# Kernel tuning notes

Measured on AMD Instinct MI355X. Metric: run time of the kernel, lower is better.

## Reference

```python
import jax, jax.numpy as jnp
import numpy as np

B, NT, NP = 4096, 2048, 1024
DT = 1e-3


def _cum_trap(y, dx):
    # cumulative trapezoid along last dim, zero-prepended (preserve_dims=True)
    c = jnp.cumsum((y[..., 1:] + y[..., :-1]) * (0.5 * dx), axis=-1)
    return jnp.concatenate([jnp.zeros_like(y[..., :1]), c], axis=-1)


def _trapz(y, dx):
    return jnp.sum(y[..., :-1] + y[..., 1:], axis=-1) * (0.5 * dx)


def _renorm(f, dx):
    # square-normalize so each trace integrates to 1 (valid pdf)
    sq = f * f
    return sq / _trapz(sq, dx)[..., None]


def _natural_cubic_coeffs(p, q):
    # p: [NP] uniform knots, q: [B, NP] values -> per-interval coeffs a,b,c,d [B, NP-1]
    h = p[1] - p[0]
    n = p.shape[0]
    rhs = 6.0 * (q[..., :-2] - 2.0 * q[..., 1:-1] + q[..., 2:]) / (h * h)  # [B, n-2]
    m = n - 2
    A = 4.0 * jnp.eye(m, dtype=q.dtype) + jnp.eye(m, k=1, dtype=q.dtype) + jnp.eye(m, k=-1, dtype=q.dtype)
    M_int = jnp.linalg.solve(A, rhs.T).T                      # [B, n-2]
    zero = jnp.zeros_like(q[..., :1])
    M = jnp.concatenate([zero, M_int, zero], axis=-1)          # natural BC: M0 = Mn = 0
    a = q[..., :-1]
    b = (q[..., 1:] - q[..., :-1]) / h - h * (2.0 * M[..., :-1] + M[..., 1:]) / 6.0
    c = M[..., :-1] / 2.0
    d = (M[..., 1:] - M[..., :-1]) / (6.0 * h)
    return a, b, c, d


def _spline_eval(p, coeffs, x):
    # evaluate batched natural cubic splines at x: [B, NT]
    a, b, c, d = coeffs
    idx = jnp.clip(jnp.searchsorted(p, x, side='right') - 1, 0, p.shape[0] - 2)  # [B, NT]
    s = x - p[idx]
    ag = jnp.take_along_axis(a, idx, axis=-1)
    bg = jnp.take_along_axis(b, idx, axis=-1)
    cg = jnp.take_along_axis(c, idx, axis=-1)
    dg = jnp.take_along_axis(d, idx, axis=-1)
    return ag + s * (bg + s * (cg + s * dg))


def setup_inputs() -> dict:
    key = jax.random.key(0)
    k1, k2 = jax.random.split(key)
    f = jax.random.normal(k1, (B, NT), dtype=jnp.float32)
    obs_data = jax.random.normal(k2, (B, NT), dtype=jnp.float32)
    t = jnp.arange(NT, dtype=jnp.float32) * DT
    p = jnp.linspace(0.0, 1.0, NP, dtype=jnp.float32)
    return {"f": f, "obs_data": obs_data, "t": t, "p": p}


def reference(f, obs_data, t, p):
    dt = t[1] - t[0]
    # ---- __init__: build per-trace quantile splines from obs_data ----
    obs_tilde = _renorm(obs_data, dt)                 # [B, NT] pdf
    cdf_obs = _cum_trap(obs_tilde, dt)                # [B, NT] cdf
    # true_quantile: step lookup q(p) = t[searchsorted(cdf, p)]
    idx = jax.vmap(lambda c: jnp.searchsorted(c, p))(cdf_obs)
    idx = jnp.clip(idx, 0, t.shape[0] - 1)
    q = t[idx]                                        # [B, NP]
    coeffs = _natural_cubic_coeffs(p, q)
    # ---- forward: W2 distance ----
    f_tilde = _renorm(f, dt)                          # [B, NT]
    F = _cum_trap(f_tilde, dt)                        # [B, NT] cdf of f
    off_diag = _spline_eval(p, coeffs, F)             # Q_obs(F(t)) [B, NT]
    diff = (t[None, :] - off_diag) ** 2
    integrated = _trapz(diff * f_tilde, dt)           # [B]
    return integrated.sum()
```

## Files before the change

kernel.cpp:

```cpp
#include <hip/hip_runtime.h>

#define NBATCH 4096
#define NT 2048
#define NP 1024
#define NTH 256
#define EPT 8
#define PPT 4
#define MSZ 1022
#define KT 4
#define IMGW 14

__global__ __launch_bounds__(NTH, 4) void w2loss_kernel(
    const float* __restrict__ f,
    const float* __restrict__ obs,
    float* __restrict__ partial)
{
    __shared__ float sQ[NP];
    __shared__ float sM[NP];
    __shared__ __align__(16) float sU[4096];
    __shared__ float sH[NTH];
    __shared__ float sPow[IMGW];
    __shared__ float sWSA[4], sWSB[4];
    __shared__ float sSqA[2], sSqB[2];
    __shared__ float sRed[4];

    float* sRp = sU;
    float4* sCF = reinterpret_cast<float4*>(sU);

    const int tid  = threadIdx.x;
    const int lane = tid & 63;
    const int wid  = tid >> 6;
    const int b    = blockIdx.x;
    const int base = tid * EPT;

    const float dt      = 0.001f;
    const float half_dt = 0.0005f;
    const float h       = 0.00097751710654936461f;
    const float inv_h   = 1023.0f;
    const float inv_h2  = 1046529.0f;
    const float h6      = h * (1.0f / 6.0f);
    const float ih6     = inv_h * (1.0f / 6.0f);

    const float* orow = obs + (size_t)b * NT;
    const float* frow = f   + (size_t)b * NT;
    float4 o0 = *reinterpret_cast<const float4*>(orow + base);
    float4 o1 = *reinterpret_cast<const float4*>(orow + base + 4);
    float4 g0 = *reinterpret_cast<const float4*>(frow + base);
    float4 g1 = *reinterpret_cast<const float4*>(frow + base + 4);

    if (tid < IMGW) {
        const float rho = -0.26794919243112270f;
        float v = 1.0f;
        for (int i = 0; i < tid; ++i) v *= rho;
        sPow[tid] = v;
    }
    if (tid < KT) { sRp[tid] = 0.0f; sRp[KT + MSZ + tid] = 0.0f; }

    float prefA[EPT], prefB[EPT];
    {
        float s0;
        s0 = o0.x*o0.x; prefA[0] = s0;
        s0 = o0.y*o0.y; prefA[1] = prefA[0] + s0;
        s0 = o0.z*o0.z; prefA[2] = prefA[1] + s0;
        s0 = o0.w*o0.w; prefA[3] = prefA[2] + s0;
        s0 = o1.x*o1.x; prefA[4] = prefA[3] + s0;
        s0 = o1.y*o1.y; prefA[5] = prefA[4] + s0;
        s0 = o1.z*o1.z; prefA[6] = prefA[5] + s0;
        s0 = o1.w*o1.w; prefA[7] = prefA[6] + s0;
        s0 = g0.x*g0.x; prefB[0] = s0;
        s0 = g0.y*g0.y; prefB[1] = prefB[0] + s0;
        s0 = g0.z*g0.z; prefB[2] = prefB[1] + s0;
        s0 = g0.w*g0.w; prefB[3] = prefB[2] + s0;
        s0 = g1.x*g1.x; prefB[4] = prefB[3] + s0;
        s0 = g1.y*g1.y; prefB[5] = prefB[4] + s0;
        s0 = g1.z*g1.z; prefB[6] = prefB[5] + s0;
        s0 = g1.w*g1.w; prefB[7] = prefB[6] + s0;
    }
    float sqA7 = o1.w * o1.w;
    float sqB7 = g1.w * g1.w;
    sH[tid] = sqA7;

    float tsA = prefA[EPT - 1], tsB = prefB[EPT - 1];
    float wsA = tsA, wsB = tsB;
#pragma unroll
    for (int off = 1; off < 64; off <<= 1) {
        float uA = __shfl_up(wsA, off);
        float uB = __shfl_up(wsB, off);
        if (lane >= off) { wsA += uA; wsB += uB; }
    }
    if (lane == 63) { sWSA[wid] = wsA; sWSB[wid] = wsB; }
    if (tid == 0)       { sSqA[0] = prefA[0]; sSqB[0] = prefB[0]; }
    if (tid == NTH - 1) { sSqA[1] = sqA7;     sSqB[1] = sqB7; }
    __syncthreads();

    float exclA = wsA - tsA, exclB = wsB - tsB;
    if (wid > 0) { exclA += sWSA[0]; exclB += sWSB[0]; }
    if (wid > 1) { exclA += sWSA[1]; exclB += sWSB[1]; }
    if (wid > 2) { exclA += sWSA[2]; exclB += sWSB[2]; }
    float totA = sWSA[0] + sWSA[1] + sWSA[2] + sWSA[3];
    float totB = sWSB[0] + sWSB[1] + sWSB[2] + sWSB[3];
    float sq0A = sSqA[0], sq0B = sSqB[0];
    float invSA = 1.0f / (half_dt * (2.0f * totA - sSqA[1] - sq0A));
    float invSB = 1.0f / (half_dt * (2.0f * totB - sSqB[1] - sq0B));

    {
        float cm;
        if (tid == 0) cm = -1.0f;
        else {
            float sqprev = sH[tid - 1];
            cm = half_dt * (((exclA - sqprev) + exclA) - sq0A) * invSA;
        }
        float Pm = exclA;
#pragma unroll
        for (int e = 0; e < EPT; ++e) {
            int j = base + e;
            float Pj = exclA + prefA[e];
            float cc = (j == 0) ? 0.0f : half_dt * (Pm + Pj - sq0A) * invSA;
            int kLo = (int)floorf(cm * inv_h) + 1;
            int kHi = (int)floorf(cc * inv_h);
            if (kLo < 0) kLo = 0;
            if (j == NT - 1) kHi = NP - 1;
            else {
                if (e == EPT - 1) kHi += 1;
                if (kHi > NP - 1) kHi = NP - 1;
            }
            float qv = (float)j * dt;
            for (int k = kLo; k <= kHi; ++k) sQ[k] = qv;
            cm = cc;
            Pm = Pj;
        }
    }
    __syncthreads();

#pragma unroll
    for (int kk = 0; kk < PPT; ++kk) {
        int i = tid + kk * NTH;
        if (i < MSZ)
            sRp[KT + i] = 6.0f * (sQ[i] - 2.0f * sQ[i + 1] + sQ[i + 2]) * inv_h2;
    }
    __syncthreads();

    {
        const float Cg = 0.28867513459481288f;
        const float CP[KT + 1] = {
            1.0f, -0.26794919243112270f, 0.071796769724490830f,
            -0.019237886466840586f, 0.0051547761428899979f };
#pragma unroll
        for (int kk = 0; kk < PPT; ++kk) {
            int i = tid + kk * NTH;
            if (i < MSZ) {
                float acc = 0.0f;
#pragma unroll
                for (int d = -KT; d <= KT; ++d) {
                    int ad = d < 0 ? -d : d;
                    acc += CP[ad] * sRp[KT + i + d];
                }
                if (i + 1 < IMGW) {
                    float t1 = 0.0f;
#pragma unroll
                    for (int k2 = 0; k2 < IMGW - 1; ++k2) t1 += sPow[k2 + 1] * sRp[KT + k2];
                    acc -= sPow[i + 1] * t1;
                }
                if (MSZ - i < IMGW) {
                    float t2 = 0.0f;
#pragma unroll
                    for (int k2 = MSZ - IMGW + 1; k2 < MSZ; ++k2) t2 += sPow[MSZ - k2] * sRp[KT + k2];
                    acc -= sPow[MSZ - i] * t2;
                }
                sM[i + 1] = Cg * acc;
            }
        }
    }
    if (tid == 0) { sM[0] = 0.0f; sM[NP - 1] = 0.0f; }
    __syncthreads();

#pragma unroll
    for (int kk = 0; kk < PPT; ++kk) {
        int k = tid + kk * NTH;
        if (k < NP - 1) {
            float a  = sQ[k];
            float qn = sQ[k + 1];
            float Mk = sM[k];
            float Mn = sM[k + 1];
            float4 cf;
            cf.x = a;
            cf.y = (qn - a) * inv_h - (2.0f * Mk + Mn) * h6;
            cf.z = 0.5f * Mk;
            cf.w = (Mn - Mk) * ih6;
            sCF[k] = cf;
        }
    }
    __syncthreads();

    float local = 0.0f;
    float term0 = 0.0f, term7 = 0.0f;
    {
        const float c1B = half_dt * invSB;
        const float K0  = (2.0f * exclB - sq0B) * c1B;
        float tj = (float)base * dt;
#pragma unroll
        for (int e = 0; e < EPT; ++e) {
            float Gj = (e ? prefB[e - 1] : 0.0f) + prefB[e];
            float Fj = __builtin_fmaf(Gj, c1B, K0);
            float sqe = e ? (prefB[e] - prefB[e - 1]) : prefB[0];
            float kf = Fj * inv_h;
            kf = fminf(fmaxf(kf, 0.0f), 1022.0f);
            int k = (int)kf;
            float s = __builtin_fmaf(-h, (float)k, Fj);
            float4 cf = sCF[k];
            float od = cf.x + s * (cf.y + s * (cf.z + s * cf.w));
            float dd = tj - od;
            float term = dd * dd * sqe;
            local += term;
            if (e == 0) term0 = term;
            if (e == EPT - 1) term7 = term;
            tj += dt;
        }
    }
    if (tid == 0)       local -= 0.5f * term0;
    if (tid == NTH - 1) local -= 0.5f * term7;

#pragma unroll
    for (int off = 32; off > 0; off >>= 1) local += __shfl_down(local, off);
    if (lane == 0) sRed[wid] = local;
    __syncthreads();
    if (tid == 0) partial[b] = (sRed[0] + sRed[1] + sRed[2] + sRed[3]) * (dt * invSB);
}

__global__ __launch_bounds__(NTH) void w2loss_reduce(
    const float* __restrict__ partial, float* __restrict__ out)
{
    __shared__ float sRed[4];
    const int tid  = threadIdx.x;
    const int lane = tid & 63;
    const int wid  = tid >> 6;
    float s = 0.0f;
#pragma unroll
    for (int i = 0; i < 16; i += 4) {
        float4 v = *reinterpret_cast<const float4*>(partial + tid * 16 + i);
        s += v.x + v.y + v.z + v.w;
    }
#pragma unroll
    for (int off = 32; off > 0; off >>= 1) s += __shfl_down(s, off);
    if (lane == 0) sRed[wid] = s;
    __syncthreads();
    if (tid == 0) out[0] = sRed[0] + sRed[1] + sRed[2] + sRed[3];
}

extern "C" void kernel_launch(void* const* d_in, const int* in_sizes, int n_in,
                              void* d_out, int out_size, void* d_ws, size_t ws_size,
                              hipStream_t stream) {
    const float* f   = (const float*)d_in[0];
    const float* obs = (const float*)d_in[1];
    float* out     = (float*)d_out;
    float* partial = (float*)d_ws;

    w2loss_kernel<<<NBATCH, NTH, 0, stream>>>(f, obs, partial);
    w2loss_reduce<<<1, NTH, 0, stream>>>(partial, out);
}
```

Baseline: 29.01 us.

## Fuse spline RHS, solve, and coefficient stages into register-tiled pass

```diff
diff --git a/kernel.cpp b/kernel.cpp
--- a/kernel.cpp
+++ b/kernel.cpp
@@ -5,27 +5,25 @@
 #define NP 1024
 #define NTH 256
 #define EPT 8
-#define PPT 4
 #define MSZ 1022
 #define KT 4
 #define IMGW 14
 
-__global__ __launch_bounds__(NTH, 4) void w2loss_kernel(
+__device__ __forceinline__ int pQ(int x) { return x + (x >> 3) + 9; }
+__device__ __forceinline__ int pM(int x) { return x + (x >> 3); }
+
+__global__ __launch_bounds__(NTH, 2) void w2loss_kernel(
     const float* __restrict__ f,
     const float* __restrict__ obs,
     float* __restrict__ partial)
 {
-    __shared__ float sQ[NP];
-    __shared__ float sM[NP];
-    __shared__ __align__(16) float sU[4096];
+    __shared__ float sQp[1168];
+    __shared__ float sMp[1152];
     __shared__ float sH[NTH];
     __shared__ float sPow[IMGW];
     __shared__ float sWSA[4], sWSB[4];
     __shared__ float sSqA[2], sSqB[2];
     __shared__ float sRed[4];
-
-    float* sRp = sU;
-    float4* sCF = reinterpret_cast<float4*>(sU);
 
     const int tid  = threadIdx.x;
     const int lane = tid & 63;
@@ -54,7 +52,6 @@
         for (int i = 0; i < tid; ++i) v *= rho;
         sPow[tid] = v;
     }
-    if (tid < KT) { sRp[tid] = 0.0f; sRp[KT + MSZ + tid] = 0.0f; }
 
     float prefA[EPT], prefB[EPT];
     {
@@ -125,18 +122,10 @@
                 if (kHi > NP - 1) kHi = NP - 1;
             }
             float qv = (float)j * dt;
-            for (int k = kLo; k <= kHi; ++k) sQ[k] = qv;
+            for (int k = kLo; k <= kHi; ++k) sQp[pQ(k)] = qv;
             cm = cc;
             Pm = Pj;
         }
-    }
-    __syncthreads();
-
-#pragma unroll
-    for (int kk = 0; kk < PPT; ++kk) {
-        int i = tid + kk * NTH;
-        if (i < MSZ)
-            sRp[KT + i] = 6.0f * (sQ[i] - 2.0f * sQ[i + 1] + sQ[i + 2]) * inv_h2;
     }
     __syncthreads();
 
@@ -145,49 +134,56 @@
         const float CP[KT + 1] = {
             1.0f, -0.26794919243112270f, 0.071796769724490830f,
             -0.019237886466840586f, 0.0051547761428899979f };
-#pragma unroll
-        for (int kk = 0; kk < PPT; ++kk) {
-            int i = tid + kk * NTH;
-            if (i < MSZ) {
-                float acc = 0.0f;
-#pragma unroll
-                for (int d = -KT; d <= KT; ++d) {
-                    int ad = d < 0 ? -d : d;
-                    acc += CP[ad] * sRp[KT + i + d];
-                }
-                if (i + 1 < IMGW) {
-                    float t1 = 0.0f;
-#pragma unroll
-                    for (int k2 = 0; k2 < IMGW - 1; ++k2) t1 += sPow[k2 + 1] * sRp[KT + k2];
-                    acc -= sPow[i + 1] * t1;
-                }
-                if (MSZ - i < IMGW) {
-                    float t2 = 0.0f;
-#pragma unroll
-                    for (int k2 = MSZ - IMGW + 1; k2 < MSZ; ++k2) t2 += sPow[MSZ - k2] * sRp[KT + k2];
-                    acc -= sPow[MSZ - i] * t2;
-                }
-                sM[i + 1] = Cg * acc;
-            }
-        }
-    }
-    if (tid == 0) { sM[0] = 0.0f; sM[NP - 1] = 0.0f; }
-    __syncthreads();
-
-#pragma unroll
-    for (int kk = 0; kk < PPT; ++kk) {
-        int k = tid + kk * NTH;
-        if (k < NP - 1) {
-            float a  = sQ[k];
-            float qn = sQ[k + 1];
-            float Mk = sM[k];
-            float Mn = sM[k + 1];
-            float4 cf;
-            cf.x = a;
-            cf.y = (qn - a) * inv_h - (2.0f * Mk + Mn) * h6;
-            cf.z = 0.5f * Mk;
-            cf.w = (Mn - Mk) * ih6;
-            sCF[k] = cf;
+        const int k0 = tid * 4;
+
+        float qw[14];
+#pragma unroll
+        for (int x = 0; x < 14; ++x) qw[x] = sQp[pQ(k0 - 5 + x)];
+
+        float r[12];
+#pragma unroll
+        for (int x = 0; x < 12; ++x) {
+            int gi = k0 - 5 + x;
+            float v = 6.0f * (qw[x] - 2.0f * qw[x + 1] + qw[x + 2]) * inv_h2;
+            r[x] = (gi >= 0 && gi < MSZ) ? v : 0.0f;
+        }
+
+        float T1 = 0.0f, T2 = 0.0f;
+        if (tid < 4) {
+            float qe[15];
+#pragma unroll
+            for (int x = 0; x < 15; ++x) qe[x] = sQp[pQ(x)];
+#pragma unroll
+            for (int x = 0; x < IMGW - 1; ++x) {
+                float rr = 6.0f * (qe[x] - 2.0f * qe[x + 1] + qe[x + 2]) * inv_h2;
+                T1 += sPow[x + 1] * rr;
+            }
+        }
+        if (tid >= NTH - 4) {
+            float qe[15];
+#pragma unroll
+            for (int x = 0; x < 15; ++x) qe[x] = sQp[pQ(1009 + x)];
+#pragma unroll
+            for (int x = 0; x < IMGW - 1; ++x) {
+                float rr = 6.0f * (qe[x] - 2.0f * qe[x + 1] + qe[x + 2]) * inv_h2;
+                T2 += sPow[13 - x] * rr;
+            }
+        }
+
+#pragma unroll
+        for (int e = 0; e < 4; ++e) {
+            int k = k0 + e;
+            float acc = 0.0f;
+#pragma unroll
+            for (int d = -KT; d <= KT; ++d) {
+                int ad = d < 0 ? -d : d;
+                acc += CP[ad] * r[e + 4 + d];
+            }
+            if (k < IMGW)        acc -= sPow[k] * T1;
+            if (1023 - k < IMGW) acc -= sPow[1023 - k] * T2;
+            float mv = Cg * acc;
+            if (k == 0 || k == NP - 1) mv = 0.0f;
+            sMp[pM(k)] = mv;
         }
     }
     __syncthreads();
@@ -207,9 +203,13 @@
             kf = fminf(fmaxf(kf, 0.0f), 1022.0f);
             int k = (int)kf;
             float s = __builtin_fmaf(-h, (float)k, Fj);
-            float4 cf = sCF[k];
-            float od = cf.x + s * (cf.y + s * (cf.z + s * cf.w));
-            float dd = tj - od;
+            float q0 = sQp[pQ(k)];
+            float q1 = sQp[pQ(k + 1)];
+            float M0 = sMp[pM(k)];
+            float M1 = sMp[pM(k + 1)];
+            float bco = (q1 - q0) * inv_h - (2.0f * M0 + M1) * h6;
+            float od  = q0 + s * (bco + s * (0.5f * M0 + s * (M1 - M0) * ih6));
+            float dd  = tj - od;
             float term = dd * dd * sqe;
             local += term;
             if (e == 0) term0 = term;
```

Measured after the change: 32.25 us. 1.11x slower.

## Fuse spline coefficient build into evaluation and pad shared arrays

Applied to the files above, without the earlier changes.

```diff
diff --git a/kernel.cpp b/kernel.cpp
--- a/kernel.cpp
+++ b/kernel.cpp
@@ -10,22 +10,21 @@
 #define KT 4
 #define IMGW 14
 
-__global__ __launch_bounds__(NTH, 4) void w2loss_kernel(
+__device__ __forceinline__ int pI(int x) { return x + (x >> 3); }
+
+__global__ __launch_bounds__(NTH, 8) void w2loss_kernel(
     const float* __restrict__ f,
     const float* __restrict__ obs,
     float* __restrict__ partial)
 {
-    __shared__ float sQ[NP];
-    __shared__ float sM[NP];
-    __shared__ __align__(16) float sU[4096];
+    __shared__ float sQp[1156];
+    __shared__ float sMp[1156];
+    __shared__ float sRp[MSZ + 2 * KT];
     __shared__ float sH[NTH];
     __shared__ float sPow[IMGW];
     __shared__ float sWSA[4], sWSB[4];
     __shared__ float sSqA[2], sSqB[2];
     __shared__ float sRed[4];
-
-    float* sRp = sU;
-    float4* sCF = reinterpret_cast<float4*>(sU);
 
     const int tid  = threadIdx.x;
     const int lane = tid & 63;
@@ -125,7 +124,7 @@
                 if (kHi > NP - 1) kHi = NP - 1;
             }
             float qv = (float)j * dt;
-            for (int k = kLo; k <= kHi; ++k) sQ[k] = qv;
+            for (int k = kLo; k <= kHi; ++k) sQp[pI(k)] = qv;
             cm = cc;
             Pm = Pj;
         }
@@ -136,7 +135,7 @@
     for (int kk = 0; kk < PPT; ++kk) {
         int i = tid + kk * NTH;
         if (i < MSZ)
-            sRp[KT + i] = 6.0f * (sQ[i] - 2.0f * sQ[i + 1] + sQ[i + 2]) * inv_h2;
+            sRp[KT + i] = 6.0f * (sQp[pI(i)] - 2.0f * sQp[pI(i + 1)] + sQp[pI(i + 2)]) * inv_h2;
     }
     __syncthreads();
 
@@ -167,29 +166,11 @@
                     for (int k2 = MSZ - IMGW + 1; k2 < MSZ; ++k2) t2 += sPow[MSZ - k2] * sRp[KT + k2];
                     acc -= sPow[MSZ - i] * t2;
                 }
-                sM[i + 1] = Cg * acc;
+                sMp[pI(i + 1)] = Cg * acc;
             }
         }
     }
-    if (tid == 0) { sM[0] = 0.0f; sM[NP - 1] = 0.0f; }
-    __syncthreads();
-
-#pragma unroll
-    for (int kk = 0; kk < PPT; ++kk) {
-        int k = tid + kk * NTH;
-        if (k < NP - 1) {
-            float a  = sQ[k];
-            float qn = sQ[k + 1];
-            float Mk = sM[k];
-            float Mn = sM[k + 1];
-            float4 cf;
-            cf.x = a;
-            cf.y = (qn - a) * inv_h - (2.0f * Mk + Mn) * h6;
-            cf.z = 0.5f * Mk;
-            cf.w = (Mn - Mk) * ih6;
-            sCF[k] = cf;
-        }
-    }
+    if (tid == 0) { sMp[pI(0)] = 0.0f; sMp[pI(NP - 1)] = 0.0f; }
     __syncthreads();
 
     float local = 0.0f;
@@ -207,9 +188,13 @@
             kf = fminf(fmaxf(kf, 0.0f), 1022.0f);
             int k = (int)kf;
             float s = __builtin_fmaf(-h, (float)k, Fj);
-            float4 cf = sCF[k];
-            float od = cf.x + s * (cf.y + s * (cf.z + s * cf.w));
-            float dd = tj - od;
+            float q0 = sQp[pI(k)];
+            float q1 = sQp[pI(k + 1)];
+            float M0 = sMp[pI(k)];
+            float M1 = sMp[pI(k + 1)];
+            float bco = (q1 - q0) * inv_h - (2.0f * M0 + M1) * h6;
+            float od  = q0 + s * (bco + s * (0.5f * M0 + s * (M1 - M0) * ih6));
+            float dd  = tj - od;
             float term = dd * dd * sqe;
             local += term;
             if (e == 0) term0 = term;
```

Measured after the change: 30.71 us. +5.9%, slower.
